# Kernel optimization log

Measured on AMD Instinct MI355X. Metric: run time of the kernel, lower is better.

The kernel has to match this reference:

```python
import jax, jax.numpy as jnp
import numpy as np

DIAG_MASK = 1e20  # value added on the diagonal to exclude self as negative


def setup_inputs() -> dict:
    key = jax.random.key(0)
    k1, k2, k3 = jax.random.split(key, 3)
    B, D_in, D_out = 4096, 1024, 1024
    anchor_x = jax.random.normal(k1, (B, D_in), dtype=jnp.float32)
    pos_x = jax.random.normal(k2, (B, D_in), dtype=jnp.float32)
    W = jax.random.normal(k3, (D_in, D_out), dtype=jnp.float32) * (1.0 / np.sqrt(D_in))
    b = jnp.zeros((D_out,), dtype=jnp.float32)
    return {"anchor_x": anchor_x, "pos_x": pos_x, "W": W, "b": b}


def reference(anchor_x, pos_x, W, b):
    # Encoder: simple dense projection (stand-in for the wrapped BERT encoder).
    anchor = anchor_x @ W + b          # [B, D]
    pos = pos_x @ W + b                # [B, D]

    # Pairwise squared distances dist[i,j] = ||anchor_i - pos_j||^2,
    # computed via the GEMM identity |a|^2 + |p|^2 - 2 a.p (same math as the
    # original broadcasted (a_i - p_j)^2 reduce_sum, far less memory traffic).
    a2 = jnp.sum(anchor * anchor, axis=-1, keepdims=True)       # [B, 1]
    p2 = jnp.sum(pos * pos, axis=-1, keepdims=True).T           # [1, B]
    dist = a2 + p2 - 2.0 * (anchor @ pos.T)                     # [B, B]

    B = dist.shape[0]
    mask_dist = dist + jnp.eye(B, dtype=dist.dtype) * DIAG_MASK  # mask diagonal
    indices = jnp.argmin(mask_dist, axis=-1)                     # [B] hard negatives
    neg = pos[indices]                                           # gather [B, D]

    return jnp.concatenate([anchor, pos, neg], axis=-1)          # [B, 3D]
```

## Files before the change

### kernel.cpp

```cpp
#include <hip/hip_runtime.h>


typedef short s8v __attribute__((ext_vector_type(8)));
typedef _Float16 h8v __attribute__((ext_vector_type(8)));
typedef float f4v __attribute__((ext_vector_type(4)));
typedef unsigned short u16;

#define B  4096
#define D  1024
#define OLD 3072
#define OLD16 6144
#define LDK 68

__device__ __forceinline__ u16 f2bf(float f) {
  union { float f; unsigned u; } v; v.f = f;
  unsigned r = v.u + 0x7FFFu + ((v.u >> 16) & 1u);
  return (u16)(r >> 16);
}
__device__ __forceinline__ float bf2f(u16 s) {
  union { unsigned u; float f; } v; v.u = ((unsigned)s) << 16;
  return v.f;
}

__device__ __forceinline__ void gld16(const void* g, void* l) {
  __builtin_amdgcn_global_load_lds(
      (const __attribute__((address_space(1))) unsigned int*)g,
      (__attribute__((address_space(3))) unsigned int*)l, 16, 0, 0);
}

__device__ __forceinline__ unsigned ldsaddr(const void* p) {
  const __attribute__((address_space(3))) char* lp =
      (const __attribute__((address_space(3))) char*)p;
  unsigned a;
  __builtin_memcpy(&a, &lp, 4);
  return a;
}

struct Top2 { float v1, v2; int j1, j2; };
__device__ __forceinline__ void t2_insert(Top2& t, float v, int j) {
  if (v < t.v1 || (v == t.v1 && j < t.j1)) {
    t.v2 = t.v1; t.j2 = t.j1; t.v1 = v; t.j1 = j;
  } else if (v < t.v2 || (v == t.v2 && j < t.j2)) {
    t.v2 = v; t.j2 = j;
  }
}
struct Top4 { float v[4]; int j[4]; };
__device__ __forceinline__ void t4_insert(Top4& t, float v, int j) {
  if (v < t.v[3] || (v == t.v[3] && j < t.j[3])) {
    int p = 3;
#pragma unroll
    for (int s = 0; s < 3; ++s) {
      if (p > 0 && (v < t.v[p - 1] || (v == t.v[p - 1] && j < t.j[p - 1]))) {
        t.v[p] = t.v[p - 1]; t.j[p] = t.j[p - 1]; --p;
      }
    }
    t.v[p] = v; t.j[p] = j;
  }
}

__global__ __launch_bounds__(256) void split_all(
    const float* __restrict__ A, const float* __restrict__ P,
    const float* __restrict__ W, u16* __restrict__ O16,
    u16* __restrict__ posXq, u16* __restrict__ WtQ, float* __restrict__ p2) {
  __shared__ float tile[32][33];
  const int bb = blockIdx.x, tid = threadIdx.x;
  if (bb < 2 * B) {
    const bool isPos = bb >= B;
    const int row = isPos ? bb - B : bb;
    const float4 v = *(const float4*)&(isPos ? P : A)[(size_t)row * D + tid * 4];
    const float vv[4] = {v.x, v.y, v.z, v.w};
    ushort4 hi, mi;
    u16* hp = &hi.x; u16* mp = &mi.x;
#pragma unroll
    for (int i = 0; i < 4; ++i) {
      hp[i] = f2bf(vv[i]);
      mp[i] = f2bf(vv[i] - bf2f(hp[i]));
    }
    if (isPos) {
      *(ushort4*)&posXq[(size_t)row * 2048 + tid * 4] = hi;
      *(ushort4*)&posXq[(size_t)row * 2048 + 1024 + tid * 4] = mi;
      if (tid == 0) p2[row] = 0.0f;
    } else {
      *(ushort4*)&O16[(size_t)row * OLD16 + 4096 + tid * 4] = hi;
      *(ushort4*)&O16[(size_t)row * OLD16 + 5120 + tid * 4] = mi;
    }
  } else {
    const int b2 = bb - 2 * B;
    const int bx = (b2 & 31) * 32, by = (b2 >> 5) * 32;
    const int tx = tid & 31, ty = tid >> 5;
    for (int dy = 0; dy < 32; dy += 8)
      tile[ty + dy][tx] = W[(size_t)(by + ty + dy) * D + bx + tx];
    __syncthreads();
    for (int dy = 0; dy < 32; dy += 8) {
      const float v = tile[tx][ty + dy];
      const u16 h = f2bf(v);
      const size_t o = (size_t)(bx + ty + dy) * 2048 + by + tx;
      WtQ[o] = h;
      WtQ[o + 1024] = f2bf(v - bf2f(h));
    }
  }
}

__global__ __launch_bounds__(256) void enc_mfma(
    float* out, const u16* __restrict__ posXq, const u16* __restrict__ WtQ,
    const float* __restrict__ bias, _Float16* __restrict__ Aq,
    _Float16* __restrict__ Pq, float* __restrict__ p2) {
  __shared__ __align__(16) u16 lAh[4][128 * 32], lAm[4][128 * 32];
  __shared__ __align__(16) u16 lBh[4][128 * 32], lBm[4][128 * 32];
  const u16* O16 = (const u16*)out;
  const int tid = threadIdx.x, lane = tid & 63, wave = tid >> 6;
  const int waveM = wave >> 1, waveN = wave & 1;
  const int row16 = lane & 15, quad = lane >> 4;
  const int g = blockIdx.x + (blockIdx.y << 3);
  const int bx = (g >> 3) & 7;
  const int by = (g & 7) | ((g >> 6) << 3);
  const bool isPos = by >= 32;
  const int Mbase = (by & 31) * 128;
  const int Nbase = bx * 128;
  f4v acc[4][4] = {};
  const int slot = (quad ^ ((row16 >> 1) & 3)) * 8;

  auto STAGE = [&](int buf, int kk) {
#pragma unroll
    for (int i = 0; i < 2; ++i) {
      const int c = i * 256 + tid;
      const int row = c >> 2;
      const int col8 = ((c & 3) ^ ((row >> 1) & 3)) * 8;
      const int lo = (i * 256 + wave * 64) * 8;
      if (isPos) {
        gld16(&posXq[(size_t)(Mbase + row) * 2048 + kk + col8], &lAh[buf][lo]);
        gld16(&posXq[(size_t)(Mbase + row) * 2048 + 1024 + kk + col8], &lAm[buf][lo]);
      } else {
        gld16(&O16[(size_t)(Mbase + row) * OLD16 + 4096 + kk + col8], &lAh[buf][lo]);
        gld16(&O16[(size_t)(Mbase + row) * OLD16 + 5120 + kk + col8], &lAm[buf][lo]);
      }
      gld16(&WtQ[(size_t)(Nbase + row) * 2048 + kk + col8], &lBh[buf][lo]);
      gld16(&WtQ[(size_t)(Nbase + row) * 2048 + 1024 + kk + col8], &lBm[buf][lo]);
    }
  };

  STAGE(0, 0);
  STAGE(1, 32);
  for (int t = 0; t < 32; ++t) {
    if (t + 2 < 32) STAGE((t + 2) & 3, (t + 2) * 32);
    if (t < 30)       asm volatile("s_waitcnt vmcnt(16)" ::: "memory");
    else if (t == 30) asm volatile("s_waitcnt vmcnt(8)" ::: "memory");
    else              asm volatile("s_waitcnt vmcnt(0)" ::: "memory");
    __builtin_amdgcn_sched_barrier(0);
    __builtin_amdgcn_s_barrier();
    __builtin_amdgcn_sched_barrier(0);
    const int cur = t & 3;
    s8v ah[4], am[4], bh[4], bm[4];
#pragma unroll
    for (int mi = 0; mi < 4; ++mi) {
      const int ro = (waveM * 64 + mi * 16 + row16) * 32 + slot;
      ah[mi] = *(const s8v*)&lAh[cur][ro];
      am[mi] = *(const s8v*)&lAm[cur][ro];
    }
#pragma unroll
    for (int ni = 0; ni < 4; ++ni) {
      const int ro = (waveN * 64 + ni * 16 + row16) * 32 + slot;
      bh[ni] = *(const s8v*)&lBh[cur][ro];
      bm[ni] = *(const s8v*)&lBm[cur][ro];
    }
    __builtin_amdgcn_s_setprio(1);
#pragma unroll
    for (int mi = 0; mi < 4; ++mi)
#pragma unroll
      for (int ni = 0; ni < 4; ++ni) {
        f4v a = acc[mi][ni];
        a = __builtin_amdgcn_mfma_f32_16x16x32_bf16(ah[mi], bh[ni], a, 0, 0, 0);
        a = __builtin_amdgcn_mfma_f32_16x16x32_bf16(ah[mi], bm[ni], a, 0, 0, 0);
        a = __builtin_amdgcn_mfma_f32_16x16x32_bf16(am[mi], bh[ni], a, 0, 0, 0);
        acc[mi][ni] = a;
      }
    __builtin_amdgcn_s_setprio(0);
  }
  const int outOff = isPos ? 1024 : 0;
  _Float16* Q = isPos ? Pq : Aq;
  float bv4[4];
#pragma unroll
  for (int ni = 0; ni < 4; ++ni)
    bv4[ni] = bias[Nbase + waveN * 64 + ni * 16 + row16];
#pragma unroll
  for (int mi = 0; mi < 4; ++mi) {
    const int rbase = Mbase + waveM * 64 + mi * 16 + quad * 4;
#pragma unroll
    for (int r = 0; r < 4; ++r) {
      const size_t row = rbase + r;
      float ss = 0.0f;
#pragma unroll
      for (int ni = 0; ni < 4; ++ni) {
        const int col = Nbase + waveN * 64 + ni * 16 + row16;
        const float v = acc[mi][ni][r] + bv4[ni];
        out[row * OLD + outOff + col] = v;
        Q[row * 1024 + col] = (_Float16)v;
        ss += v * v;
      }
      if (isPos) {
        ss += __shfl_xor(ss, 1, 64);
        ss += __shfl_xor(ss, 2, 64);
        ss += __shfl_xor(ss, 4, 64);
        ss += __shfl_xor(ss, 8, 64);
        if (row16 == 0) atomicAdd(&p2[row], ss);
      }
    }
  }
}

__global__ __launch_bounds__(256) void pnorm(float* __restrict__ o) {
  const int row = blockIdx.x, t = threadIdx.x;
  const float4 v = *(const float4*)&o[(size_t)row * OLD + D + t * 4];
  float s = v.x * v.x + v.y * v.y + v.z * v.z + v.w * v.w;
#pragma unroll
  for (int off = 32; off; off >>= 1) s += __shfl_down(s, off, 64);
  __shared__ float wsum[4];
  if ((t & 63) == 0) wsum[t >> 6] = s;
  __syncthreads();
  if (t == 0) o[(size_t)row * OLD + 2048] = wsum[0] + wsum[1] + wsum[2] + wsum[3];
}

__global__ __launch_bounds__(512, 2) void dist_mfma(
    const _Float16* __restrict__ Aq, const _Float16* __restrict__ Pq,
    const float* __restrict__ p2, float* __restrict__ o) {
  __shared__ __align__(16) u16 lA[4][256 * 32];
  __shared__ __align__(16) u16 lB[4][256 * 32];
  const int tid = threadIdx.x, lane = tid & 63, wave = tid >> 6;
  const int waveM = wave >> 2, waveN = wave & 3;
  const int row16 = lane & 15, quad = lane >> 4;
  const int Mbase = blockIdx.y * 256;
  const int Nbase = blockIdx.x * 256;
  f4v acc[8][4] = {};

  auto STAGE = [&](int buf, int kk) {
#pragma unroll
    for (int i = 0; i < 2; ++i) {
      const int c = i * 512 + tid;
      const int row = c >> 2;
      const int col8 = ((c & 3) ^ ((row >> 1) & 3)) * 8;
      u16* la = &lA[buf][(i * 512 + wave * 64) * 8];
      u16* lb = &lB[buf][(i * 512 + wave * 64) * 8];
      gld16(&Aq[(size_t)(Mbase + row) * 1024 + kk + col8], la);
      gld16(&Pq[(size_t)(Nbase + row) * 1024 + kk + col8], lb);
    }
  };

  STAGE(0, 0);
  STAGE(1, 32);
  const int slot = (quad ^ ((row16 >> 1) & 3)) * 8;
  const unsigned aoff = (unsigned)(((waveM * 128 + row16) * 32 + slot) * 2);
  const unsigned boff = (unsigned)(((waveN * 64 + row16) * 32 + slot) * 2);
  const unsigned lA0 = ldsaddr(&lA[0][0]);
  const unsigned lB0 = ldsaddr(&lB[0][0]);
  for (int t = 0; t < 32; ++t) {
    if (t + 2 < 32) STAGE((t + 2) & 3, (t + 2) * 32);
    if (t < 30)       asm volatile("s_waitcnt vmcnt(8)" ::: "memory");
    else if (t == 30) asm volatile("s_waitcnt vmcnt(4)" ::: "memory");
    else              asm volatile("s_waitcnt vmcnt(0)" ::: "memory");
    __builtin_amdgcn_sched_barrier(0);
    __builtin_amdgcn_s_barrier();
    __builtin_amdgcn_sched_barrier(0);
    const int cur = t & 3;
    const unsigned abase = lA0 + (unsigned)cur * 16384 + aoff;
    const unsigned bbase = lB0 + (unsigned)cur * 16384 + boff;
    h8v a[8], b[4];
#pragma unroll
    for (int mi = 0; mi < 8; ++mi) {
      const unsigned av = abase + (unsigned)mi * 1024;
      asm volatile("ds_read_b128 %0, %1" : "=v"(a[mi]) : "v"(av));
    }
#pragma unroll
    for (int ni = 0; ni < 4; ++ni) {
      const unsigned bv = bbase + (unsigned)ni * 1024;
      asm volatile("ds_read_b128 %0, %1" : "=v"(b[ni]) : "v"(bv));
    }
    __builtin_amdgcn_sched_barrier(0);
    asm volatile("s_waitcnt lgkmcnt(0)" ::: "memory");
    __builtin_amdgcn_sched_barrier(0);
    __builtin_amdgcn_s_setprio(1);
#pragma unroll
    for (int mi = 0; mi < 8; ++mi)
#pragma unroll
      for (int ni = 0; ni < 4; ++ni)
        acc[mi][ni] =
            __builtin_amdgcn_mfma_f32_16x16x32_f16(a[mi], b[ni], acc[mi][ni], 0, 0, 0);
    __builtin_amdgcn_s_setprio(0);
  }
  __syncthreads();

  float (*sv1)[4] = (float(*)[4])&lA[0][0];
  float (*sv2)[4] = (float(*)[4])((char*)&lA[0][0] + 4096);
  int   (*sj1)[4] = (int(*)[4])((char*)&lA[0][0] + 8192);
  int   (*sj2)[4] = (int(*)[4])((char*)&lA[0][0] + 12288);

  float p2c[4];
#pragma unroll
  for (int ni = 0; ni < 4; ++ni)
    p2c[ni] = p2[Nbase + waveN * 64 + ni * 16 + row16];
#pragma unroll
  for (int mi = 0; mi < 8; ++mi)
#pragma unroll
    for (int r = 0; r < 4; ++r) {
      const int rg = Mbase + waveM * 128 + mi * 16 + quad * 4 + r;
      Top2 tp; tp.v1 = 3.0e38f; tp.v2 = 3.0e38f; tp.j1 = 0; tp.j2 = 1;
#pragma unroll
      for (int ni = 0; ni < 4; ++ni) {
        const int cg = Nbase + waveN * 64 + ni * 16 + row16;
        if (cg != rg) t2_insert(tp, p2c[ni] - 2.0f * acc[mi][ni][r], cg);
      }
#pragma unroll
      for (int m = 1; m < 16; m <<= 1) {
        const float ov1 = __shfl_xor(tp.v1, m, 64);
        const int oj1 = __shfl_xor(tp.j1, m, 64);
        const float ov2 = __shfl_xor(tp.v2, m, 64);
        const int oj2 = __shfl_xor(tp.j2, m, 64);
        t2_insert(tp, ov1, oj1);
        t2_insert(tp, ov2, oj2);
      }
      if (row16 == 0) {
        const int rl = waveM * 128 + mi * 16 + quad * 4 + r;
        sv1[rl][waveN] = tp.v1; sj1[rl][waveN] = tp.j1;
        sv2[rl][waveN] = tp.v2; sj2[rl][waveN] = tp.j2;
      }
    }
  __syncthreads();
  if (tid < 256) {
    Top2 tp; tp.v1 = sv1[tid][0]; tp.j1 = sj1[tid][0];
    tp.v2 = sv2[tid][0]; tp.j2 = sj2[tid][0];
#pragma unroll
    for (int w = 1; w < 4; ++w) {
      t2_insert(tp, sv1[tid][w], sj1[tid][w]);
      t2_insert(tp, sv2[tid][w], sj2[tid][w]);
    }
    ((float4*)&o[(size_t)(Mbase + tid) * OLD + 2056])[blockIdx.x] =
        make_float4(tp.v1, __int_as_float(tp.j1), tp.v2, __int_as_float(tp.j2));
  }
}

__global__ __launch_bounds__(256) void argmin_refine(float* __restrict__ o) {
  const int i = blockIdx.x, t = threadIdx.x;
  __shared__ int gj[4];
  if (t < 64) {
    Top4 tp;
#pragma unroll
    for (int c = 0; c < 4; ++c) { tp.v[c] = 3.0e38f; tp.j[c] = 0; }
    if (t < 16) {
      const float4 p = ((const float4*)&o[(size_t)i * OLD + 2056])[t];
      t4_insert(tp, p.x, __float_as_int(p.y));
      t4_insert(tp, p.z, __float_as_int(p.w));
    }
#pragma unroll
    for (int m = 1; m < 32; m <<= 1) {
#pragma unroll
      for (int c = 0; c < 4; ++c) {
        const float ov = __shfl_xor(tp.v[c], m, 64);
        const int oj = __shfl_xor(tp.j[c], m, 64);
        t4_insert(tp, ov, oj);
      }
    }
    if (t == 0) {
#pragma unroll
      for (int c = 0; c < 4; ++c)
        gj[c] = (tp.j[c] < 0) ? 0 : (tp.j[c] > B - 1 ? B - 1 : tp.j[c]);
    }
  }
  __syncthreads();
  int jj[4];
#pragma unroll
  for (int c = 0; c < 4; ++c) jj[c] = gj[c];
  const float4 a4 = *(const float4*)&o[(size_t)i * OLD + t * 4];
  float s[4], n[4];
#pragma unroll
  for (int c = 0; c < 4; ++c) {
    const float4 q = *(const float4*)&o[(size_t)jj[c] * OLD + D + t * 4];
    s[c] = a4.x * q.x + a4.y * q.y + a4.z * q.z + a4.w * q.w;
    n[c] = q.x * q.x + q.y * q.y + q.z * q.z + q.w * q.w;
  }
#pragma unroll
  for (int off = 32; off; off >>= 1)
#pragma unroll
    for (int c = 0; c < 4; ++c) {
      s[c] += __shfl_down(s[c], off, 64);
      n[c] += __shfl_down(n[c], off, 64);
    }
  __shared__ float wsum[4][8];
  __shared__ int sjf;
  if ((t & 63) == 0)
#pragma unroll
    for (int c = 0; c < 4; ++c) {
      wsum[t >> 6][c] = s[c];
      wsum[t >> 6][4 + c] = n[c];
    }
  __syncthreads();
  if (t == 0) {
    float bd = 3.4e38f; int bj = 0x7fffffff;
#pragma unroll
    for (int c = 0; c < 4; ++c) {
      const float S = wsum[0][c] + wsum[1][c] + wsum[2][c] + wsum[3][c];
      const float N = wsum[0][4 + c] + wsum[1][4 + c] + wsum[2][4 + c] + wsum[3][4 + c];
      const float d = N - 2.0f * S;
      const int j = jj[c];
      if (d < bd || (d == bd && j < bj)) { bd = d; bj = j; }
    }
    sjf = bj;
  }
  __syncthreads();
  const int j = sjf;
  ((float4*)&o[(size_t)i * OLD + 2048])[t] = ((const float4*)&o[(size_t)j * OLD + D])[t];
}

__global__ __launch_bounds__(256) void enc_gemm(
    const float* __restrict__ X, const float* __restrict__ W,
    const float* __restrict__ bia, float* __restrict__ out, int outOff) {
  __shared__ float lA[32][LDK];
  __shared__ float lW[32][LDK];
  const int tid = threadIdx.x;
  const int Mbase = blockIdx.y * 64;
  const int Nbase = blockIdx.x * 64;
  const int ty = tid >> 4, tx = tid & 15;
  float acc[4][4] = {};
  for (int k0 = 0; k0 < D; k0 += 32) {
    __syncthreads();
#pragma unroll
    for (int h = 0; h < 2; ++h) {
      const int ch = tid + h * 256;
      const int r = ch >> 3, c4 = (ch & 7) * 4;
      const float4 a4 = *(const float4*)&X[(size_t)(Mbase + r) * D + k0 + c4];
      lA[c4 + 0][r] = a4.x; lA[c4 + 1][r] = a4.y;
      lA[c4 + 2][r] = a4.z; lA[c4 + 3][r] = a4.w;
      const int kr = ch >> 4, nc = (ch & 15) * 4;
      *(float4*)&lW[kr][nc] = *(const float4*)&W[(size_t)(k0 + kr) * D + Nbase + nc];
    }
    __syncthreads();
#pragma unroll
    for (int kk = 0; kk < 32; ++kk) {
      const float4 av = *(const float4*)&lA[kk][ty * 4];
      const float4 wv = *(const float4*)&lW[kk][tx * 4];
      acc[0][0] += av.x * wv.x; acc[0][1] += av.x * wv.y; acc[0][2] += av.x * wv.z; acc[0][3] += av.x * wv.w;
      acc[1][0] += av.y * wv.x; acc[1][1] += av.y * wv.y; acc[1][2] += av.y * wv.z; acc[1][3] += av.y * wv.w;
      acc[2][0] += av.z * wv.x; acc[2][1] += av.z * wv.y; acc[2][2] += av.z * wv.z; acc[2][3] += av.z * wv.w;
      acc[3][0] += av.w * wv.x; acc[3][1] += av.w * wv.y; acc[3][2] += av.w * wv.z; acc[3][3] += av.w * wv.w;
    }
  }
  const float4 b4 = *(const float4*)&bia[Nbase + tx * 4];
#pragma unroll
  for (int i = 0; i < 4; ++i) {
    const int row = Mbase + ty * 4 + i;
    float4 ov;
    ov.x = acc[i][0] + b4.x; ov.y = acc[i][1] + b4.y;
    ov.z = acc[i][2] + b4.z; ov.w = acc[i][3] + b4.w;
    *(float4*)&out[(size_t)row * OLD + outOff + Nbase + tx * 4] = ov;
  }
}

__global__ __launch_bounds__(256) void dist_argmin_f32(float* __restrict__ o) {
  __shared__ float lA[32][LDK];
  __shared__ float lB[32][LDK];
  const int tid = threadIdx.x;
  const int Mbase = blockIdx.y * 64, Nbase = blockIdx.x * 64;
  const int ty = tid >> 4, tx = tid & 15;
  float acc[4][4] = {};
  for (int k0 = 0; k0 < D; k0 += 32) {
    __syncthreads();
#pragma unroll
    for (int h = 0; h < 2; ++h) {
      const int ch = tid + h * 256;
      const int r = ch >> 3, c4 = (ch & 7) * 4;
      const float4 a4 = *(const float4*)&o[(size_t)(Mbase + r) * OLD + k0 + c4];
      const float4 b4 = *(const float4*)&o[(size_t)(Nbase + r) * OLD + D + k0 + c4];
      lA[c4 + 0][r] = a4.x; lA[c4 + 1][r] = a4.y;
      lA[c4 + 2][r] = a4.z; lA[c4 + 3][r] = a4.w;
      lB[c4 + 0][r] = b4.x; lB[c4 + 1][r] = b4.y;
      lB[c4 + 2][r] = b4.z; lB[c4 + 3][r] = b4.w;
    }
    __syncthreads();
#pragma unroll
    for (int kk = 0; kk < 32; ++kk) {
      const float4 av = *(const float4*)&lA[kk][ty * 4];
      const float4 bv = *(const float4*)&lB[kk][tx * 4];
      acc[0][0] += av.x * bv.x; acc[0][1] += av.x * bv.y; acc[0][2] += av.x * bv.z; acc[0][3] += av.x * bv.w;
      acc[1][0] += av.y * bv.x; acc[1][1] += av.y * bv.y; acc[1][2] += av.y * bv.z; acc[1][3] += av.y * bv.w;
      acc[2][0] += av.z * bv.x; acc[2][1] += av.z * bv.y; acc[2][2] += av.z * bv.z; acc[2][3] += av.z * bv.w;
      acc[3][0] += av.w * bv.x; acc[3][1] += av.w * bv.y; acc[3][2] += av.w * bv.z; acc[3][3] += av.w * bv.w;
    }
  }
  float colp2[4];
#pragma unroll
  for (int j = 0; j < 4; ++j)
    colp2[j] = o[(size_t)(Nbase + tx * 4 + j) * OLD + 2048];
#pragma unroll
  for (int i = 0; i < 4; ++i) {
    const int rg = Mbase + ty * 4 + i;
    float bv = 3.0e38f; int bj = 0;
#pragma unroll
    for (int j = 0; j < 4; ++j) {
      const int cg = Nbase + tx * 4 + j;
      const float d = colp2[j] - 2.0f * acc[i][j];
      if (cg != rg && d < bv) { bv = d; bj = cg; }
    }
#pragma unroll
    for (int m = 1; m < 16; m <<= 1) {
      const float ov = __shfl_xor(bv, m, 64);
      const int oj = __shfl_xor(bj, m, 64);
      if (ov < bv || (ov == bv && oj < bj)) { bv = ov; bj = oj; }
    }
    if (tx == 0)
      ((float2*)&o[(size_t)rg * OLD + 2056])[blockIdx.x] =
          make_float2(bv, __int_as_float(bj));
  }
}

__global__ __launch_bounds__(256) void argmin_final_f2(float* __restrict__ o, int nblk) {
  const int i = blockIdx.x, t = threadIdx.x;
  __shared__ int sj;
  if (t < 64) {
    float v = 3.4e38f; int j = 0x7fffffff;
    if (t < nblk) {
      const float2 p = ((const float2*)&o[(size_t)i * OLD + 2056])[t];
      v = p.x; j = __float_as_int(p.y);
    }
#pragma unroll
    for (int m = 32; m; m >>= 1) {
      const float ov = __shfl_xor(v, m, 64);
      const int oj = __shfl_xor(j, m, 64);
      if (ov < v || (ov == v && oj < j)) { v = ov; j = oj; }
    }
    if (t == 0) sj = (j < 0) ? 0 : (j > B - 1 ? B - 1 : j);
  }
  __syncthreads();
  const int j = sj;
  ((float4*)&o[(size_t)i * OLD + 2048])[t] = ((const float4*)&o[(size_t)j * OLD + D])[t];
}

extern "C" void kernel_launch(void* const* d_in, const int* in_sizes, int n_in,
                              void* d_out, int out_size, void* d_ws, size_t ws_size,
                              hipStream_t stream) {
  const float* anchor_x = (const float*)d_in[0];
  const float* pos_x    = (const float*)d_in[1];
  const float* W        = (const float*)d_in[2];
  const float* b        = (const float*)d_in[3];
  float* out = (float*)d_out;
  char* ws = (char*)d_ws;
  const size_t MB = 1024 * 1024;

  if (ws_size >= 37 * MB) {
    _Float16* Aq = (_Float16*)(ws);
    _Float16* Pq = (_Float16*)(ws + 8 * MB);
    u16* WtQ     = (u16*)(ws + 16 * MB);
    u16* posXq   = (u16*)(ws + 20 * MB);
    float* p2    = (float*)(ws + 36 * MB);
    split_all<<<2 * B + 1024, 256, 0, stream>>>(anchor_x, pos_x, W,
                                                (u16*)out, posXq, WtQ, p2);
    enc_mfma<<<dim3(8, 64), 256, 0, stream>>>(out, posXq, WtQ, b, Aq, Pq, p2);
    dist_mfma<<<dim3(16, 16), 512, 0, stream>>>(Aq, Pq, p2, out);
    argmin_refine<<<B, 256, 0, stream>>>(out);
  } else {
    enc_gemm<<<dim3(16, 64), 256, 0, stream>>>(anchor_x, W, b, out, 0);
    enc_gemm<<<dim3(16, 64), 256, 0, stream>>>(pos_x,    W, b, out, 1024);
    pnorm<<<B, 256, 0, stream>>>(out);
    dist_argmin_f32<<<dim3(64, 64), 256, 0, stream>>>(out);
    argmin_final_f2<<<B, 256, 0, stream>>>(out, 64);
  }
}
```

Before: 298.9 us.

## Shrink distance GEMM tile to 256x128 with 4 waves and double grid

```diff
diff --git a/kernel.cpp b/kernel.cpp
--- a/kernel.cpp
+++ b/kernel.cpp
@@ -26,14 +26,6 @@
   __builtin_amdgcn_global_load_lds(
       (const __attribute__((address_space(1))) unsigned int*)g,
       (__attribute__((address_space(3))) unsigned int*)l, 16, 0, 0);
-}
-
-__device__ __forceinline__ unsigned ldsaddr(const void* p) {
-  const __attribute__((address_space(3))) char* lp =
-      (const __attribute__((address_space(3))) char*)p;
-  unsigned a;
-  __builtin_memcpy(&a, &lp, 4);
-  return a;
 }
 
 struct Top2 { float v1, v2; int j1, j2; };
@@ -220,63 +212,56 @@
   if (t == 0) o[(size_t)row * OLD + 2048] = wsum[0] + wsum[1] + wsum[2] + wsum[3];
 }
 
-__global__ __launch_bounds__(512, 2) void dist_mfma(
+__global__ __launch_bounds__(256) void dist_mfma(
     const _Float16* __restrict__ Aq, const _Float16* __restrict__ Pq,
     const float* __restrict__ p2, float* __restrict__ o) {
   __shared__ __align__(16) u16 lA[4][256 * 32];
-  __shared__ __align__(16) u16 lB[4][256 * 32];
+  __shared__ __align__(16) u16 lB[4][128 * 32];
   const int tid = threadIdx.x, lane = tid & 63, wave = tid >> 6;
-  const int waveM = wave >> 2, waveN = wave & 3;
+  const int waveM = wave >> 1, waveN = wave & 1;
   const int row16 = lane & 15, quad = lane >> 4;
   const int Mbase = blockIdx.y * 256;
-  const int Nbase = blockIdx.x * 256;
+  const int Nbase = blockIdx.x * 128;
   f4v acc[8][4] = {};
+  const int slot = (quad ^ ((row16 >> 1) & 3)) * 8;
 
   auto STAGE = [&](int buf, int kk) {
 #pragma unroll
-    for (int i = 0; i < 2; ++i) {
-      const int c = i * 512 + tid;
+    for (int i = 0; i < 4; ++i) {
+      const int c = i * 256 + tid;
       const int row = c >> 2;
       const int col8 = ((c & 3) ^ ((row >> 1) & 3)) * 8;
-      u16* la = &lA[buf][(i * 512 + wave * 64) * 8];
-      u16* lb = &lB[buf][(i * 512 + wave * 64) * 8];
-      gld16(&Aq[(size_t)(Mbase + row) * 1024 + kk + col8], la);
-      gld16(&Pq[(size_t)(Nbase + row) * 1024 + kk + col8], lb);
+      gld16(&Aq[(size_t)(Mbase + row) * 1024 + kk + col8],
+            &lA[buf][(i * 256 + wave * 64) * 8]);
+    }
+#pragma unroll
+    for (int i = 0; i < 2; ++i) {
+      const int c = i * 256 + tid;
+      const int row = c >> 2;
+      const int col8 = ((c & 3) ^ ((row >> 1) & 3)) * 8;
+      gld16(&Pq[(size_t)(Nbase + row) * 1024 + kk + col8],
+            &lB[buf][(i * 256 + wave * 64) * 8]);
     }
   };
 
   STAGE(0, 0);
   STAGE(1, 32);
-  const int slot = (quad ^ ((row16 >> 1) & 3)) * 8;
-  const unsigned aoff = (unsigned)(((waveM * 128 + row16) * 32 + slot) * 2);
-  const unsigned boff = (unsigned)(((waveN * 64 + row16) * 32 + slot) * 2);
-  const unsigned lA0 = ldsaddr(&lA[0][0]);
-  const unsigned lB0 = ldsaddr(&lB[0][0]);
   for (int t = 0; t < 32; ++t) {
     if (t + 2 < 32) STAGE((t + 2) & 3, (t + 2) * 32);
-    if (t < 30)       asm volatile("s_waitcnt vmcnt(8)" ::: "memory");
-    else if (t == 30) asm volatile("s_waitcnt vmcnt(4)" ::: "memory");
+    if (t < 30)       asm volatile("s_waitcnt vmcnt(12)" ::: "memory");
+    else if (t == 30) asm volatile("s_waitcnt vmcnt(6)" ::: "memory");
     else              asm volatile("s_waitcnt vmcnt(0)" ::: "memory");
     __builtin_amdgcn_sched_barrier(0);
     __builtin_amdgcn_s_barrier();
     __builtin_amdgcn_sched_barrier(0);
     const int cur = t & 3;
-    const unsigned abase = lA0 + (unsigned)cur * 16384 + aoff;
-    const unsigned bbase = lB0 + (unsigned)cur * 16384 + boff;
     h8v a[8], b[4];
 #pragma unroll
-    for (int mi = 0; mi < 8; ++mi) {
-      const unsigned av = abase + (unsigned)mi * 1024;
-      asm volatile("ds_read_b128 %0, %1" : "=v"(a[mi]) : "v"(av));
-    }
-#pragma unroll
-    for (int ni = 0; ni < 4; ++ni) {
-      const unsigned bv = bbase + (unsigned)ni * 1024;
-      asm volatile("ds_read_b128 %0, %1" : "=v"(b[ni]) : "v"(bv));
-    }
-    __builtin_amdgcn_sched_barrier(0);
-    asm volatile("s_waitcnt lgkmcnt(0)" ::: "memory");
-    __builtin_amdgcn_sched_barrier(0);
+    for (int mi = 0; mi < 8; ++mi)
+      a[mi] = *(const h8v*)&lA[cur][(waveM * 128 + mi * 16 + row16) * 32 + slot];
+#pragma unroll
+    for (int ni = 0; ni < 4; ++ni)
+      b[ni] = *(const h8v*)&lB[cur][(waveN * 64 + ni * 16 + row16) * 32 + slot];
     __builtin_amdgcn_s_setprio(1);
 #pragma unroll
     for (int mi = 0; mi < 8; ++mi)
@@ -288,10 +273,10 @@
   }
   __syncthreads();
 
-  float (*sv1)[4] = (float(*)[4])&lA[0][0];
-  float (*sv2)[4] = (float(*)[4])((char*)&lA[0][0] + 4096);
-  int   (*sj1)[4] = (int(*)[4])((char*)&lA[0][0] + 8192);
-  int   (*sj2)[4] = (int(*)[4])((char*)&lA[0][0] + 12288);
+  float (*sv1)[2] = (float(*)[2])&lA[0][0];
+  float (*sv2)[2] = (float(*)[2])((char*)&lA[0][0] + 2048);
+  int   (*sj1)[2] = (int(*)[2])((char*)&lA[0][0] + 4096);
+  int   (*sj2)[2] = (int(*)[2])((char*)&lA[0][0] + 6144);
 
   float p2c[4];
 #pragma unroll
@@ -324,14 +309,11 @@
       }
     }
   __syncthreads();
-  if (tid < 256) {
+  {
     Top2 tp; tp.v1 = sv1[tid][0]; tp.j1 = sj1[tid][0];
     tp.v2 = sv2[tid][0]; tp.j2 = sj2[tid][0];
-#pragma unroll
-    for (int w = 1; w < 4; ++w) {
-      t2_insert(tp, sv1[tid][w], sj1[tid][w]);
-      t2_insert(tp, sv2[tid][w], sj2[tid][w]);
-    }
+    t2_insert(tp, sv1[tid][1], sj1[tid][1]);
+    t2_insert(tp, sv2[tid][1], sj2[tid][1]);
     ((float4*)&o[(size_t)(Mbase + tid) * OLD + 2056])[blockIdx.x] =
         make_float4(tp.v1, __int_as_float(tp.j1), tp.v2, __int_as_float(tp.j2));
   }
@@ -344,7 +326,7 @@
     Top4 tp;
 #pragma unroll
     for (int c = 0; c < 4; ++c) { tp.v[c] = 3.0e38f; tp.j[c] = 0; }
-    if (t < 16) {
+    if (t < 32) {
       const float4 p = ((const float4*)&o[(size_t)i * OLD + 2056])[t];
       t4_insert(tp, p.x, __float_as_int(p.y));
       t4_insert(tp, p.z, __float_as_int(p.w));
@@ -552,7 +534,7 @@
     split_all<<<2 * B + 1024, 256, 0, stream>>>(anchor_x, pos_x, W,
                                                 (u16*)out, posXq, WtQ, p2);
     enc_mfma<<<dim3(8, 64), 256, 0, stream>>>(out, posXq, WtQ, b, Aq, Pq, p2);
-    dist_mfma<<<dim3(16, 16), 512, 0, stream>>>(Aq, Pq, p2, out);
+    dist_mfma<<<dim3(32, 16), 256, 0, stream>>>(Aq, Pq, p2, out);
     argmin_refine<<<B, 256, 0, stream>>>(out);
   } else {
     enc_gemm<<<dim3(16, 64), 256, 0, stream>>>(anchor_x, W, b, out, 0);
```

New measurement: 502.4 us. 1.68x slower.
